# Optimization experiments

Measured on AMD Instinct MI355X. Metric: run time of the kernel, lower is better.

## Reference

```python
import jax, jax.numpy as jnp
import numpy as np

N = 100000
E = 1600000
IN_FEATS = 128
OUT_FEATS = 32


def setup_inputs() -> dict:
    key = jax.random.key(0)
    k1, k2, k3, k4, k5, k6 = jax.random.split(key, 6)
    features = jax.random.normal(k1, (N, IN_FEATS), dtype=jnp.float32)
    src = jax.random.randint(k2, (E,), 0, N, dtype=jnp.int32)
    dst = jax.random.randint(k3, (E,), 0, N, dtype=jnp.int32)
    # xavier_normal-like scale for fc_weight, attn vectors
    gain = float(np.sqrt(2.0))  # calculate_gain('relu')
    fc_std = gain * np.sqrt(2.0 / (IN_FEATS + OUT_FEATS))
    at_std = gain * np.sqrt(2.0 / (1 + OUT_FEATS))
    fc_weight = jax.random.normal(k4, (IN_FEATS, OUT_FEATS), dtype=jnp.float32) * fc_std
    attn_l = jax.random.normal(k5, (OUT_FEATS,), dtype=jnp.float32) * at_std
    attn_r = jax.random.normal(k6, (OUT_FEATS,), dtype=jnp.float32) * at_std
    return {"features": features, "src": src, "dst": dst,
            "fc_weight": fc_weight, "attn_l": attn_l, "attn_r": attn_r}


def reference(features, src, dst, fc_weight, attn_l, attn_r):
    # dense projection: [N, out]
    h = features @ fc_weight
    # per-node attention logits (GSDDMM operands)
    el = (h * attn_l).sum(-1)  # [N]
    er = (h * attn_r).sum(-1)  # [N]
    # SDDMM: edge score = el[u] + er[v], LeakyReLU(0.2)
    e = jax.nn.leaky_relu(el[src] + er[dst], negative_slope=0.2)  # [E]
    # edge softmax over destination node
    m = jax.ops.segment_max(e, dst, num_segments=N)  # [N], -inf for isolated nodes
    m = jnp.where(jnp.isfinite(m), m, 0.0)
    ex = jnp.exp(e - m[dst])
    s = jax.ops.segment_sum(ex, dst, num_segments=N)  # [N]
    alpha = ex / s[dst]  # [E]
    # SpMM: out[v] = sum_{(u,v) in E} h[u] * alpha[(u,v)]
    out = jax.ops.segment_sum(h[src] * alpha[:, None], dst, num_segments=N)  # [N, out]
    return out
```

## Files before the change

kernel.cpp:

```cpp
#include <hip/hip_runtime.h>
#include <math.h>

#define IN_FEATS 128
#define OUT_FEATS 32
#define BSHIFT 8
#define NPB 256
#define KMAX 512
#define CHUNK 4096
#define PEPT 8
#define CAPL 5120

__device__ __forceinline__ unsigned short f2bf(float f) {
    unsigned int u = __float_as_uint(f);
    u += 0x7FFFu + ((u >> 16) & 1u);
    return (unsigned short)(u >> 16);
}
__device__ __forceinline__ float bf2f_lo(unsigned int v) {
    return __uint_as_float(v << 16);
}
__device__ __forceinline__ float bf2f_hi(unsigned int v) {
    return __uint_as_float(v & 0xFFFF0000u);
}

__global__ __launch_bounds__(256) void proj_kernel(
    const float* __restrict__ features,
    const float* __restrict__ W,
    const float* __restrict__ attn_l,
    const float* __restrict__ attn_r,
    unsigned short* __restrict__ h,
    float* __restrict__ el,
    float* __restrict__ er,
    int N)
{
    __shared__ float Ws[IN_FEATS * OUT_FEATS];
    __shared__ float featT[4][IN_FEATS][16];

    const int t  = threadIdx.x;
    const int n0 = blockIdx.x * 64;

    {
        const float4* Wg = (const float4*)W;
        float4* Wl = (float4*)Ws;
#pragma unroll
        for (int i = 0; i < 4; ++i)
            Wl[t + 256 * i] = Wg[t + 256 * i];
    }

    {
        const int r = t >> 2;
        const int q = t & 3;
        const int wbuf = r >> 4;
        const int nl   = r & 15;
        if (n0 + r < N) {
            const float* frow = features + (size_t)(n0 + r) * IN_FEATS;
#pragma unroll
            for (int m = 0; m < 8; ++m) {
                int c = q * 8 + m;
                float4 f4 = *(const float4*)(frow + c * 4);
                featT[wbuf][c * 4 + 0][nl] = f4.x;
                featT[wbuf][c * 4 + 1][nl] = f4.y;
                featT[wbuf][c * 4 + 2][nl] = f4.z;
                featT[wbuf][c * 4 + 3][nl] = f4.w;
            }
        }
    }
    __syncthreads();

    const int wv   = t >> 6;
    const int lane = t & 63;
    const int jq   = lane & 7;
    const int ns   = lane >> 3;

    float4 acc0 = make_float4(0.f, 0.f, 0.f, 0.f);
    float4 acc1 = make_float4(0.f, 0.f, 0.f, 0.f);

#pragma unroll 16
    for (int k = 0; k < IN_FEATS; ++k) {
        float4 w4 = *(const float4*)&Ws[k * OUT_FEATS + jq * 4];
        float2 f2 = *(const float2*)&featT[wv][k][ns * 2];
        acc0.x += f2.x * w4.x; acc0.y += f2.x * w4.y;
        acc0.z += f2.x * w4.z; acc0.w += f2.x * w4.w;
        acc1.x += f2.y * w4.x; acc1.y += f2.y * w4.y;
        acc1.z += f2.y * w4.z; acc1.w += f2.y * w4.w;
    }

    const int node0 = n0 + wv * 16 + ns * 2;
    const float4 al4 = ((const float4*)attn_l)[jq];
    const float4 ar4 = ((const float4*)attn_r)[jq];

    float pl0 = acc0.x * al4.x + acc0.y * al4.y + acc0.z * al4.z + acc0.w * al4.w;
    float pr0 = acc0.x * ar4.x + acc0.y * ar4.y + acc0.z * ar4.z + acc0.w * ar4.w;
    float pl1 = acc1.x * al4.x + acc1.y * al4.y + acc1.z * al4.z + acc1.w * al4.w;
    float pr1 = acc1.x * ar4.x + acc1.y * ar4.y + acc1.z * ar4.z + acc1.w * ar4.w;
#pragma unroll
    for (int off = 1; off < 8; off <<= 1) {
        pl0 += __shfl_xor(pl0, off);
        pr0 += __shfl_xor(pr0, off);
        pl1 += __shfl_xor(pl1, off);
        pr1 += __shfl_xor(pr1, off);
    }

    if (node0 < N) {
        ushort4 p;
        p.x = f2bf(acc0.x); p.y = f2bf(acc0.y); p.z = f2bf(acc0.z); p.w = f2bf(acc0.w);
        *(ushort4*)(h + (size_t)node0 * OUT_FEATS + jq * 4) = p;
        if (jq == 0) { el[node0] = pl0; er[node0] = pr0; }
    }
    if (node0 + 1 < N) {
        ushort4 p;
        p.x = f2bf(acc1.x); p.y = f2bf(acc1.y); p.z = f2bf(acc1.z); p.w = f2bf(acc1.w);
        *(ushort4*)(h + (size_t)(node0 + 1) * OUT_FEATS + jq * 4) = p;
        if (jq == 0) { el[node0 + 1] = pl1; er[node0 + 1] = pr1; }
    }
}

__global__ __launch_bounds__(512) void init_cursor_kernel(
    int* __restrict__ gcursor, int K, int region)
{
    int b = blockIdx.x * blockDim.x + threadIdx.x;
    if (b < K) gcursor[b] = b * region;
}

__global__ __launch_bounds__(512) void partition_kernel(
    const int* __restrict__ src,
    const int* __restrict__ dst,
    int* __restrict__ gcursor,
    int* __restrict__ binned,
    int E, int region)
{
    __shared__ int hist[KMAX];
    __shared__ int lbase[KMAX];
    __shared__ int rnk[KMAX];
    int t = threadIdx.x;
    if (t < KMAX) { hist[t] = 0; rnk[t] = 0; }
    __syncthreads();

    int base = blockIdx.x * CHUNK;
    int s_reg[PEPT], d_reg[PEPT];
#pragma unroll
    for (int i = 0; i < PEPT; ++i) {
        int idx = base + i * 512 + t;
        if (idx < E) {
            s_reg[i] = src[idx];
            d_reg[i] = dst[idx];
            atomicAdd(&hist[d_reg[i] >> BSHIFT], 1);
        } else d_reg[i] = -1;
    }
    __syncthreads();
    if (t < KMAX && hist[t] > 0) lbase[t] = atomicAdd(&gcursor[t], hist[t]);
    __syncthreads();
#pragma unroll
    for (int i = 0; i < PEPT; ++i) {
        if (d_reg[i] >= 0) {
            int b = d_reg[i] >> BSHIFT;
            int pos = lbase[b] + atomicAdd(&rnk[b], 1);
            if (pos < (b + 1) * region)
                binned[pos] = ((d_reg[i] & (NPB - 1)) << 17) | s_reg[i];
        }
    }
}

__global__ __launch_bounds__(1024) void bucket_agg_kernel(
    const int* __restrict__ binned,
    const int* __restrict__ gcursor,
    const unsigned short* __restrict__ h,
    const float* __restrict__ el,
    const float* __restrict__ er,
    float* __restrict__ out,
    int N, int region)
{
    __shared__ int lcnt[NPB];
    __shared__ int rowL[NPB];
    __shared__ int degL[NPB];
    __shared__ int cur[NPB];
    __shared__ int slds[CAPL];

    const int b = blockIdx.x;
    const int t = threadIdx.x;
    const int estart = b * region;
    int bucketE = gcursor[b] - estart;
    bucketE = min(bucketE, min(region, CAPL));

    if (t < NPB) lcnt[t] = 0;
    __syncthreads();

    for (int i = t; i < bucketE; i += 1024)
        atomicAdd(&lcnt[binned[estart + i] >> 17], 1);
    __syncthreads();

    int myc = (t < NPB) ? lcnt[t] : 0;
    for (int off = 1; off < NPB; off <<= 1) {
        int x = (t < NPB && t >= off) ? lcnt[t - off] : 0;
        __syncthreads();
        if (t < NPB) lcnt[t] += x;
        __syncthreads();
    }
    if (t < NPB) {
        int excl = lcnt[t] - myc;
        rowL[t] = excl;
        degL[t] = myc;
        cur[t]  = excl;
    }
    __syncthreads();

    for (int i = t; i < bucketE; i += 1024) {
        int packed = binned[estart + i];
        int pos = atomicAdd(&cur[packed >> 17], 1);
        slds[pos] = packed & 0x1FFFF;
    }
    __syncthreads();

    const int w    = t >> 6;
    const int lane = t & 63;
    const int quad = lane & 7;
    const int esub = lane >> 3;

    for (int nl = w; nl < NPB; nl += 16) {
        int node = (b << BSHIFT) + nl;
        if (node >= N) break;
        int d  = degL[nl];
        int rs = rowL[nl];

        float4 acc = make_float4(0.f, 0.f, 0.f, 0.f);
        float  s   = 0.f;
        float  er_n = (d > 0) ? er[node] : 0.f;

        for (int base = 0; base < d; base += 32) {
            int u[4];
#pragma unroll
            for (int r = 0; r < 4; ++r) {
                int i = base + esub + 8 * r;
                u[r] = (i < d) ? slds[rs + i] : -1;
            }
            float ee[4]; uint2 hh[4];
#pragma unroll
            for (int r = 0; r < 4; ++r) {
                if (u[r] >= 0) {
                    ee[r] = el[u[r]];
                    hh[r] = *(const uint2*)(h + (size_t)u[r] * OUT_FEATS + quad * 4);
                }
            }
#pragma unroll
            for (int r = 0; r < 4; ++r) {
                if (u[r] >= 0) {
                    float v = ee[r] + er_n;
                    v = (v > 0.f) ? v : 0.2f * v;
                    float a = __expf(v);
                    s += a;
                    acc.x += a * bf2f_lo(hh[r].x);
                    acc.y += a * bf2f_hi(hh[r].x);
                    acc.z += a * bf2f_lo(hh[r].y);
                    acc.w += a * bf2f_hi(hh[r].y);
                }
            }
        }
#pragma unroll
        for (int off = 8; off < 64; off <<= 1) {
            acc.x += __shfl_xor(acc.x, off);
            acc.y += __shfl_xor(acc.y, off);
            acc.z += __shfl_xor(acc.z, off);
            acc.w += __shfl_xor(acc.w, off);
            s     += __shfl_xor(s, off);
        }
        if (esub == 0) {
            float inv = (d > 0) ? 1.f / s : 0.f;
            float4 o = make_float4(acc.x * inv, acc.y * inv, acc.z * inv, acc.w * inv);
            *(float4*)(out + (size_t)node * OUT_FEATS + quad * 4) = o;
        }
    }
}

extern "C" void kernel_launch(void* const* d_in, const int* in_sizes, int n_in,
                              void* d_out, int out_size, void* d_ws, size_t ws_size,
                              hipStream_t stream)
{
    const float* features = (const float*)d_in[0];
    const int*   src      = (const int*)d_in[1];
    const int*   dst      = (const int*)d_in[2];
    const float* fc_w     = (const float*)d_in[3];
    const float* attn_l   = (const float*)d_in[4];
    const float* attn_r   = (const float*)d_in[5];

    const int N = in_sizes[0] / IN_FEATS;
    const int E = in_sizes[1];

    float* out = (float*)d_out;

    const int K = (N + NPB - 1) >> BSHIFT;
    const int reg = (E + K - 1) / K;
    int region = reg + 768;
    if (region > CAPL) region = CAPL;

    char* ws = (char*)d_ws;
    int*   binned  = (int*)ws;
    unsigned short* h = (unsigned short*)(binned + (size_t)K * region);
    float* el      = (float*)(h + (size_t)N * OUT_FEATS);
    float* er      = el + N;
    int*   gcursor = (int*)(er + N);

    proj_kernel<<<(N + 63) / 64, 256, 0, stream>>>(
        features, fc_w, attn_l, attn_r, h, el, er, N);

    init_cursor_kernel<<<(K + 511) / 512, 512, 0, stream>>>(gcursor, K, region);

    partition_kernel<<<(E + CHUNK - 1) / CHUNK, 512, 0, stream>>>(
        src, dst, gcursor, binned, E, region);

    bucket_agg_kernel<<<K, 1024, 0, stream>>>(
        binned, gcursor, h, el, er, out, N, region);
}
```

Measured before the change: 176.2 us.

## Reuse atomic ranks for binning, warp-shuffle scan, two nodes per wavefront

The partition kernel now keeps the rank returned by the histogram atomic and drops its second rank atomic pass. The bucket aggregation kernel loads its records into registers once, ranks them with one LDS atomic, and replaces the barrier-heavy Hillis-Steele scan with a wave-shuffle scan. The aggregation loop also splits each 64-lane wave into two halves, each handling one node with 16 edges per iteration. This cuts barriers, global reloads and idle lanes on low-degree nodes, at the cost of more registers and a continue in place of the early break.

```diff
diff --git a/kernel.cpp b/kernel.cpp
--- a/kernel.cpp
+++ b/kernel.cpp
@@ -9,6 +9,7 @@
 #define CHUNK 4096
 #define PEPT 8
 #define CAPL 5120
+#define RPT 5
 
 __device__ __forceinline__ unsigned short f2bf(float f) {
     unsigned int u = __float_as_uint(f);
@@ -130,20 +131,19 @@
 {
     __shared__ int hist[KMAX];
     __shared__ int lbase[KMAX];
-    __shared__ int rnk[KMAX];
     int t = threadIdx.x;
-    if (t < KMAX) { hist[t] = 0; rnk[t] = 0; }
+    if (t < KMAX) hist[t] = 0;
     __syncthreads();
 
     int base = blockIdx.x * CHUNK;
-    int s_reg[PEPT], d_reg[PEPT];
+    int s_reg[PEPT], d_reg[PEPT], r_reg[PEPT];
 #pragma unroll
     for (int i = 0; i < PEPT; ++i) {
         int idx = base + i * 512 + t;
         if (idx < E) {
             s_reg[i] = src[idx];
             d_reg[i] = dst[idx];
-            atomicAdd(&hist[d_reg[i] >> BSHIFT], 1);
+            r_reg[i] = atomicAdd(&hist[d_reg[i] >> BSHIFT], 1);
         } else d_reg[i] = -1;
     }
     __syncthreads();
@@ -153,7 +153,7 @@
     for (int i = 0; i < PEPT; ++i) {
         if (d_reg[i] >= 0) {
             int b = d_reg[i] >> BSHIFT;
-            int pos = lbase[b] + atomicAdd(&rnk[b], 1);
+            int pos = lbase[b] + r_reg[i];
             if (pos < (b + 1) * region)
                 binned[pos] = ((d_reg[i] & (NPB - 1)) << 17) | s_reg[i];
         }
@@ -172,7 +172,7 @@
     __shared__ int lcnt[NPB];
     __shared__ int rowL[NPB];
     __shared__ int degL[NPB];
-    __shared__ int cur[NPB];
+    __shared__ int wsum[4];
     __shared__ int slds[CAPL];
 
     const int b = blockIdx.x;
@@ -184,40 +184,57 @@
     if (t < NPB) lcnt[t] = 0;
     __syncthreads();
 
-    for (int i = t; i < bucketE; i += 1024)
-        atomicAdd(&lcnt[binned[estart + i] >> 17], 1);
-    __syncthreads();
-
-    int myc = (t < NPB) ? lcnt[t] : 0;
-    for (int off = 1; off < NPB; off <<= 1) {
-        int x = (t < NPB && t >= off) ? lcnt[t - off] : 0;
-        __syncthreads();
-        if (t < NPB) lcnt[t] += x;
-        __syncthreads();
-    }
+    int recs[RPT], rnk[RPT];
+#pragma unroll
+    for (int c = 0; c < RPT; ++c) {
+        int i = t + c * 1024;
+        if (i < bucketE) {
+            recs[c] = binned[estart + i];
+            rnk[c]  = atomicAdd(&lcnt[recs[c] >> 17], 1);
+        } else recs[c] = -1;
+    }
+    __syncthreads();
+
     if (t < NPB) {
-        int excl = lcnt[t] - myc;
-        rowL[t] = excl;
-        degL[t] = myc;
-        cur[t]  = excl;
-    }
-    __syncthreads();
-
-    for (int i = t; i < bucketE; i += 1024) {
-        int packed = binned[estart + i];
-        int pos = atomicAdd(&cur[packed >> 17], 1);
-        slds[pos] = packed & 0x1FFFF;
-    }
-    __syncthreads();
-
-    const int w    = t >> 6;
-    const int lane = t & 63;
-    const int quad = lane & 7;
-    const int esub = lane >> 3;
-
-    for (int nl = w; nl < NPB; nl += 16) {
+        int v = lcnt[t];
+        int x = v;
+#pragma unroll
+        for (int off = 1; off < 64; off <<= 1) {
+            int y = __shfl_up(x, off);
+            if ((t & 63) >= off) x += y;
+        }
+        if ((t & 63) == 63) wsum[t >> 6] = x;
+        degL[t] = v;
+        rowL[t] = x - v;
+    }
+    __syncthreads();
+    if (t < NPB) {
+        int wpre = 0;
+#pragma unroll
+        for (int ww = 0; ww < 4; ++ww)
+            if (ww < (t >> 6)) wpre += wsum[ww];
+        rowL[t] += wpre;
+    }
+    __syncthreads();
+
+#pragma unroll
+    for (int c = 0; c < RPT; ++c) {
+        if (recs[c] >= 0)
+            slds[rowL[recs[c] >> 17] + rnk[c]] = recs[c] & 0x1FFFF;
+    }
+    __syncthreads();
+
+    const int w     = t >> 6;
+    const int lane  = t & 63;
+    const int half  = lane >> 5;
+    const int l32   = lane & 31;
+    const int quad  = l32 & 7;
+    const int esub  = l32 >> 3;
+
+    for (int nlp = w; nlp < NPB / 2; nlp += 16) {
+        int nl   = nlp * 2 + half;
         int node = (b << BSHIFT) + nl;
-        if (node >= N) break;
+        if (node >= N) continue;
         int d  = degL[nl];
         int rs = rowL[nl];
 
@@ -225,11 +242,11 @@
         float  s   = 0.f;
         float  er_n = (d > 0) ? er[node] : 0.f;
 
-        for (int base = 0; base < d; base += 32) {
+        for (int base = 0; base < d; base += 16) {
             int u[4];
 #pragma unroll
             for (int r = 0; r < 4; ++r) {
-                int i = base + esub + 8 * r;
+                int i = base + esub + 4 * r;
                 u[r] = (i < d) ? slds[rs + i] : -1;
             }
             float ee[4]; uint2 hh[4];
@@ -255,7 +272,7 @@
             }
         }
 #pragma unroll
-        for (int off = 8; off < 64; off <<= 1) {
+        for (int off = 8; off < 32; off <<= 1) {
             acc.x += __shfl_xor(acc.x, off);
             acc.y += __shfl_xor(acc.y, off);
             acc.z += __shfl_xor(acc.z, off);
```

Result: faster. 171.9 us (-2.4%).
